# Kernel optimization log

Measured on AMD Instinct MI355X. Metric: run time of the kernel, lower is better.

## Reference

```python
import jax, jax.numpy as jnp
import numpy as np

DIM = 1024
E = 8
TOP_K = 2
HID = int(DIM * 2.68)  # 2744


def setup_inputs() -> dict:
    key = jax.random.key(0)
    ks = jax.random.split(key, 8)
    s = 0.02
    return {
        "x": jax.random.normal(ks[0], (4, 1024, DIM), dtype=jnp.float32),
        "gate_w": jax.random.normal(ks[1], (E, DIM), dtype=jnp.float32) * s,
        "w1": jax.random.normal(ks[2], (E, HID, DIM), dtype=jnp.float32) * s,
        "w2": jax.random.normal(ks[3], (E, HID, DIM), dtype=jnp.float32) * s,
        "w3": jax.random.normal(ks[4], (E, DIM, HID), dtype=jnp.float32) * s,
        "sw1": jax.random.normal(ks[5], (HID, DIM), dtype=jnp.float32) * s,
        "sw2": jax.random.normal(ks[6], (HID, DIM), dtype=jnp.float32) * s,
        "sw3": jax.random.normal(ks[7], (DIM, HID), dtype=jnp.float32) * s,
    }


def reference(x, gate_w, w1, w2, w3, sw1, sw2, sw3):
    B, T, C = x.shape
    xf = x.reshape(-1, C)  # [S, C]
    logits = xf @ gate_w.T  # [S, E]
    rw = jax.nn.softmax(logits.astype(jnp.float32), axis=-1)
    tkw, tki = jax.lax.top_k(rw, TOP_K)  # [S, K]
    nE = rw.shape[-1]
    importance = rw.mean(0)  # [E]
    load = jax.nn.one_hot(tki[:, 0], nE, dtype=jnp.float32).mean(0)  # [E]
    aux_loss = nE * (importance * load).sum()
    tkw = tkw / tkw.sum(-1, keepdims=True)
    tkw = tkw.astype(x.dtype)
    # dense all-expert SwiGLU (faithful to original: every expert on every token)
    h = jax.nn.silu(jnp.einsum('sc,ehc->seh', xf, w1)) * jnp.einsum('sc,ehc->seh', xf, w2)  # [S,E,H]
    eo = jnp.einsum('seh,ech->sec', h, w3)  # [S, E, C]
    sel = jnp.take_along_axis(eo, tki[:, :, None], axis=1)  # [S, K, C]
    weighted = (sel * tkw[:, :, None]).sum(1)  # [S, C]
    shared = (jax.nn.silu(xf @ sw1.T) * (xf @ sw2.T)) @ sw3.T  # [S, C]
    y = (weighted + shared).reshape(B, T, C)
    return y, aux_loss
```

## Files before the change

### kernel.cpp

```cpp
#include <hip/hip_runtime.h>
#include <cstdio>
#include <cstdint>

#define S_TOK 4096
#define CDIM  1024
#define EXP   8
#define HRAW  2744
#define HPAD  2816
#define MAXROWS  13312
#define MAXTILES 104
#define NSLICE1  (HPAD / 128)
#define NSLICE2  (CDIM / 128)

typedef __attribute__((ext_vector_type(8))) short bf16x8;
typedef __attribute__((ext_vector_type(4))) float f32x4;
typedef __attribute__((ext_vector_type(4))) unsigned short us4;
typedef unsigned short us;

__device__ __forceinline__ us f2bf(float f) {
  unsigned u = __float_as_uint(f);
  u += 0x7fffu + ((u >> 16) & 1u);
  return (us)(u >> 16);
}

__device__ __forceinline__ void gl16(const us* g, us* l) {
  __builtin_amdgcn_global_load_lds((__attribute__((address_space(1))) void*)g,
                                   (__attribute__((address_space(3))) void*)l,
                                   16, 0, 0);
}

__device__ __forceinline__ int xcd_swz(int orig, int nwg) {
  int q = nwg >> 3, r = nwg & 7;
  int x = orig & 7, idx = orig >> 3;
  return (x < r ? x * (q + 1) : r * (q + 1) + (x - r) * q) + idx;
}

#define CH_RP1  (HPAD * CDIM / 4)
#define CH_CPR  (HPAD / 4)
#define R_W1    (8 * CH_RP1)
#define R_W2    (R_W1 + 8 * CH_RP1)
#define R_W3    (R_W2 + 8 * CDIM * CH_CPR)
#define R_SW1   (R_W3 + CH_RP1)
#define R_SW2   (R_SW1 + CH_RP1)
#define R_SW3   (R_SW2 + CDIM * CH_CPR)

__device__ __forceinline__ void cvt4_rowpad(const float* __restrict__ src,
                                            us* __restrict__ dst, int idx) {
  int m = idx / CH_RP1, rem = idx - m * CH_RP1;
  int r = rem >> 8, c4 = rem & 255;
  us4 o;
  if (r < HRAW) {
    float4 v = *(const float4*)(src + ((size_t)(m * HRAW + r) * CDIM + c4 * 4));
    o.x = f2bf(v.x); o.y = f2bf(v.y); o.z = f2bf(v.z); o.w = f2bf(v.w);
  } else { o.x = 0; o.y = 0; o.z = 0; o.w = 0; }
  *(us4*)(dst + ((size_t)(m * HPAD + r) * CDIM + c4 * 4)) = o;
}

__device__ __forceinline__ void cvt4_colpad(const float* __restrict__ src,
                                            us* __restrict__ dst, int idx) {
  int r = idx / CH_CPR, c4 = idx - r * CH_CPR;
  int c = c4 * 4;
  us4 o;
  if (c < HRAW) {
    float4 v = *(const float4*)(src + (size_t)r * HRAW + c);
    o.x = f2bf(v.x); o.y = f2bf(v.y); o.z = f2bf(v.z); o.w = f2bf(v.w);
  } else { o.x = 0; o.y = 0; o.z = 0; o.w = 0; }
  *(us4*)(dst + (size_t)r * HPAD + c) = o;
}

__global__ void __launch_bounds__(256) cvt_all_kernel(
    const float* __restrict__ w1, const float* __restrict__ w2,
    const float* __restrict__ w3, const float* __restrict__ sw1,
    const float* __restrict__ sw2, const float* __restrict__ sw3,
    us* __restrict__ w1b, us* __restrict__ w2b, us* __restrict__ w3b,
    us* __restrict__ sw1b, us* __restrict__ sw2b, us* __restrict__ sw3b) {
  for (int i = blockIdx.x * 256 + threadIdx.x; i < R_SW3; i += gridDim.x * 256) {
    if (i < R_W1)       cvt4_rowpad(w1,  w1b,  i);
    else if (i < R_W2)  cvt4_rowpad(w2,  w2b,  i - R_W1);
    else if (i < R_W3)  cvt4_colpad(w3,  w3b,  i - R_W2);
    else if (i < R_SW1) cvt4_rowpad(sw1, sw1b, i - R_W3);
    else if (i < R_SW2) cvt4_rowpad(sw2, sw2b, i - R_SW1);
    else                cvt4_colpad(sw3, sw3b, i - R_SW2);
  }
}

__global__ void __launch_bounds__(256) gate_kernel(const float* __restrict__ x,
                                                   const float* __restrict__ gw,
                                                   us* __restrict__ xb,
                                                   int* __restrict__ tki,
                                                   float* __restrict__ tkw,
                                                   float* __restrict__ probs) {
  const int wv = threadIdx.x >> 6, lane = threadIdx.x & 63;
  const int s = blockIdx.x * 4 + wv;
  const float4* xs4 = (const float4*)(x + (size_t)s * CDIM);
  float acc[8] = {0, 0, 0, 0, 0, 0, 0, 0};
#pragma unroll
  for (int j = 0; j < 4; j++) {
    float4 v = xs4[lane * 4 + j];
    int c = lane * 16 + j * 4;
    us4 ov;
    ov.x = f2bf(v.x); ov.y = f2bf(v.y); ov.z = f2bf(v.z); ov.w = f2bf(v.w);
    *(us4*)(xb + (size_t)s * CDIM + c) = ov;
#pragma unroll
    for (int ee = 0; ee < 8; ee++) {
      const float* g = gw + ee * CDIM + c;
      acc[ee] += v.x * g[0] + v.y * g[1] + v.z * g[2] + v.w * g[3];
    }
  }
#pragma unroll
  for (int ee = 0; ee < 8; ee++) {
#pragma unroll
    for (int off = 32; off > 0; off >>= 1) acc[ee] += __shfl_xor(acc[ee], off, 64);
  }
  if (lane == 0) {
    float mx = acc[0];
    for (int ee = 1; ee < 8; ee++) mx = fmaxf(mx, acc[ee]);
    float p[8], sm = 0.f;
    for (int ee = 0; ee < 8; ee++) { p[ee] = expf(acc[ee] - mx); sm += p[ee]; }
    float inv = 1.f / sm;
    for (int ee = 0; ee < 8; ee++) probs[s * 8 + ee] = p[ee] * inv;
    int i0 = 0; float b0 = p[0];
    for (int ee = 1; ee < 8; ee++) if (p[ee] > b0) { b0 = p[ee]; i0 = ee; }
    int i1 = -1; float b1 = -1.f;
    for (int ee = 0; ee < 8; ee++) if (ee != i0 && p[ee] > b1) { b1 = p[ee]; i1 = ee; }
    float rw0 = b0 * inv, rw1 = b1 * inv;
    float den = 1.f / (rw0 + rw1);
    tki[2 * s] = i0; tki[2 * s + 1] = i1;
    tkw[2 * s] = rw0 * den; tkw[2 * s + 1] = rw1 * den;
  }
}

__global__ void __launch_bounds__(512) build_kernel(const int* __restrict__ tki,
                                                    const float* __restrict__ tkw,
                                                    const float* __restrict__ probs,
                                                    int* __restrict__ meta,
                                                    int* __restrict__ pairtok,
                                                    float* __restrict__ pairw,
                                                    int* __restrict__ invmap,
                                                    int* __restrict__ tile_expert,
                                                    float* __restrict__ aux_out) {
  const int tid = threadIdx.x, lane = tid & 63, wv = tid >> 6;
  __shared__ int s_cnt[EXP];
  __shared__ int s_amc[EXP];
  __shared__ float s_imp[EXP];
  {
    const int e = wv;
    int c_cnt = 0, c_amc = 0;
    float imp = 0.f;
    for (int s0 = 0; s0 < S_TOK; s0 += 64) {
      int s = s0 + lane;
      int i0 = tki[2 * s], i1 = tki[2 * s + 1];
      c_cnt += (i0 == e) || (i1 == e);
      c_amc += (i0 == e);
      imp += probs[s * 8 + e];
    }
#pragma unroll
    for (int off = 32; off > 0; off >>= 1) {
      c_cnt += __shfl_xor(c_cnt, off, 64);
      c_amc += __shfl_xor(c_amc, off, 64);
      imp   += __shfl_xor(imp, off, 64);
    }
    if (lane == 0) { s_cnt[e] = c_cnt; s_amc[e] = c_amc; s_imp[e] = imp; }
  }
  __syncthreads();
  int pad[EXP], start[EXP];
  int o = S_TOK;
#pragma unroll
  for (int j = 0; j < EXP; j++) {
    pad[j] = ((s_cnt[j] + 127) >> 7) << 7;
    start[j] = o;
    o += pad[j];
  }
  const int total = o;
  for (int r = tid; r < S_TOK; r += 512) { pairtok[r] = r; pairw[r] = 1.f; }
  {
    const int e = wv;
    int base = start[e];
    for (int s0 = 0; s0 < S_TOK; s0 += 64) {
      int s = s0 + lane;
      int i0 = tki[2 * s], i1 = tki[2 * s + 1];
      bool m0 = (i0 == e), m1 = (i1 == e);
      bool mm = m0 || m1;
      unsigned long long mk = __ballot(mm);
      if (mm) {
        int pos = base + __popcll(mk & ((1ull << lane) - 1ull));
        pairtok[pos] = s;
        pairw[pos] = m0 ? tkw[2 * s] : tkw[2 * s + 1];
        invmap[2 * s + (m0 ? 0 : 1)] = pos;
      }
      base += __popcll(mk);
    }
    for (int r = base + lane; r < start[e] + pad[e]; r += 64) {
      pairtok[r] = -1; pairw[r] = 0.f;
    }
  }
  if (tid < 128) {
    int ex = 8;
    if (tid >= 32) {
      int rr = tid * 128;
#pragma unroll
      for (int j = 0; j < EXP; j++)
        if (rr >= start[j] && rr < start[j] + pad[j]) ex = j;
    }
    tile_expert[tid] = ex;
  }
  if (tid == 0) {
    meta[0] = total >> 7;
    float a = 0.f;
    for (int j = 0; j < EXP; j++)
      a += (s_imp[j] * (1.f / 4096.f)) * ((float)s_amc[j] * (1.f / 4096.f));
    aux_out[0] = 8.f * a;
  }
}

__global__ void __launch_bounds__(256, 2) gemm1_kernel(
    const us* __restrict__ xb, const us* __restrict__ w1b, const us* __restrict__ w2b,
    const us* __restrict__ sw1b, const us* __restrict__ sw2b,
    const int* __restrict__ pairtok, const int* __restrict__ tile_expert,
    const int* __restrict__ meta, us* __restrict__ h) {
  const int wgid = xcd_swz(blockIdx.x, MAXTILES * NSLICE1);
  const int mt = wgid % MAXTILES;
  if (mt >= meta[0]) return;
  const int n0 = (wgid / MAXTILES) * 128;
  const int e = tile_expert[mt];
  const us* B1 = (e == 8) ? sw1b : (w1b + (size_t)e * HPAD * CDIM);
  const us* B2 = (e == 8) ? sw2b : (w2b + (size_t)e * HPAD * CDIM);
  const int row0 = mt * 128;
  __shared__ __align__(16) us sA[128 * 32];
  __shared__ __align__(16) us sB1[128 * 32];
  __shared__ __align__(16) us sB2[128 * 32];
  const int tid = threadIdx.x, lane = tid & 63;
  const int wm = tid >> 7, wn = (tid >> 6) & 1;
  const int sub = tid & 3, ra = tid >> 2;
  const int subx = sub ^ ((ra >> 1) & 3);
  int t0 = pairtok[row0 + ra];      if (t0 < 0) t0 = 0;
  int t1 = pairtok[row0 + 64 + ra]; if (t1 < 0) t1 = 0;
  const us* gA0 = xb + (size_t)t0 * CDIM + subx * 8;
  const us* gA1 = xb + (size_t)t1 * CDIM + subx * 8;
  const us* gB1a = B1 + (size_t)(n0 + ra) * CDIM + subx * 8;
  const us* gB1b = B1 + (size_t)(n0 + 64 + ra) * CDIM + subx * 8;
  const us* gB2a = B2 + (size_t)(n0 + ra) * CDIM + subx * 8;
  const us* gB2b = B2 + (size_t)(n0 + 64 + ra) * CDIM + subx * 8;
  f32x4 au[4][4], av[4][4];
#pragma unroll
  for (int m = 0; m < 4; m++)
#pragma unroll
    for (int n = 0; n < 4; n++)
#pragma unroll
      for (int r = 0; r < 4; r++) { au[m][n][r] = 0.f; av[m][n][r] = 0.f; }

  const int rl = lane & 15;
  const int kx = (((lane >> 4) ^ ((lane >> 1) & 3)) << 3);
  for (int k0 = 0; k0 < CDIM; k0 += 32) {
    gl16(gA0 + k0,  &sA[tid * 8]);
    gl16(gA1 + k0,  &sA[(tid + 256) * 8]);
    gl16(gB1a + k0, &sB1[tid * 8]);
    gl16(gB1b + k0, &sB1[(tid + 256) * 8]);
    gl16(gB2a + k0, &sB2[tid * 8]);
    gl16(gB2b + k0, &sB2[(tid + 256) * 8]);
    __syncthreads();
    bf16x8 a[4], b1[4], b2[4];
#pragma unroll
    for (int m = 0; m < 4; m++)
      a[m] = *(const bf16x8*)&sA[(wm * 64 + m * 16 + rl) * 32 + kx];
#pragma unroll
    for (int n = 0; n < 4; n++) {
      b1[n] = *(const bf16x8*)&sB1[(wn * 64 + n * 16 + rl) * 32 + kx];
      b2[n] = *(const bf16x8*)&sB2[(wn * 64 + n * 16 + rl) * 32 + kx];
    }
#pragma unroll
    for (int m = 0; m < 4; m++)
#pragma unroll
      for (int n = 0; n < 4; n++) {
        au[m][n] = __builtin_amdgcn_mfma_f32_16x16x32_bf16(a[m], b1[n], au[m][n], 0, 0, 0);
        av[m][n] = __builtin_amdgcn_mfma_f32_16x16x32_bf16(a[m], b2[n], av[m][n], 0, 0, 0);
      }
    __syncthreads();
  }
  const int rb = (lane >> 4) * 4, cb = lane & 15;
#pragma unroll
  for (int m = 0; m < 4; m++)
#pragma unroll
    for (int n = 0; n < 4; n++)
#pragma unroll
      for (int r = 0; r < 4; r++) {
        int row = row0 + wm * 64 + m * 16 + rb + r;
        int col = n0 + wn * 64 + n * 16 + cb;
        float u = au[m][n][r], v = av[m][n][r];
        float sg = 1.f / (1.f + __expf(-u));
        h[(size_t)row * HPAD + col] = f2bf(u * sg * v);
      }
}

__global__ void __launch_bounds__(256, 2) gemm2_kernel(
    const us* __restrict__ h, const us* __restrict__ w3b, const us* __restrict__ sw3b,
    const int* __restrict__ tile_expert, const int* __restrict__ meta,
    float* __restrict__ eo) {
  const int wgid = xcd_swz(blockIdx.x, MAXTILES * NSLICE2);
  const int mt = wgid % MAXTILES;
  if (mt >= meta[0]) return;
  const int n0 = (wgid / MAXTILES) * 128;
  const int e = tile_expert[mt];
  const us* B = (e == 8) ? sw3b : (w3b + (size_t)e * CDIM * HPAD);
  const int row0 = mt * 128;
  __shared__ __align__(16) us sA[128 * 32];
  __shared__ __align__(16) us sB[128 * 32];
  const int tid = threadIdx.x, lane = tid & 63;
  const int wm = tid >> 7, wn = (tid >> 6) & 1;
  const int sub = tid & 3, ra = tid >> 2;
  const int subx = sub ^ ((ra >> 1) & 3);
  const us* gA0 = h + (size_t)(row0 + ra) * HPAD + subx * 8;
  const us* gA1 = h + (size_t)(row0 + 64 + ra) * HPAD + subx * 8;
  const us* gB0 = B + (size_t)(n0 + ra) * HPAD + subx * 8;
  const us* gB1 = B + (size_t)(n0 + 64 + ra) * HPAD + subx * 8;
  f32x4 ac[4][4];
#pragma unroll
  for (int m = 0; m < 4; m++)
#pragma unroll
    for (int n = 0; n < 4; n++)
#pragma unroll
      for (int r = 0; r < 4; r++) ac[m][n][r] = 0.f;

  const int rl = lane & 15;
  const int kx = (((lane >> 4) ^ ((lane >> 1) & 3)) << 3);
  for (int k0 = 0; k0 < HPAD; k0 += 32) {
    gl16(gA0 + k0, &sA[tid * 8]);
    gl16(gA1 + k0, &sA[(tid + 256) * 8]);
    gl16(gB0 + k0, &sB[tid * 8]);
    gl16(gB1 + k0, &sB[(tid + 256) * 8]);
    __syncthreads();
    bf16x8 a[4], b[4];
#pragma unroll
    for (int m = 0; m < 4; m++)
      a[m] = *(const bf16x8*)&sA[(wm * 64 + m * 16 + rl) * 32 + kx];
#pragma unroll
    for (int n = 0; n < 4; n++)
      b[n] = *(const bf16x8*)&sB[(wn * 64 + n * 16 + rl) * 32 + kx];
#pragma unroll
    for (int m = 0; m < 4; m++)
#pragma unroll
      for (int n = 0; n < 4; n++)
        ac[m][n] = __builtin_amdgcn_mfma_f32_16x16x32_bf16(a[m], b[n], ac[m][n], 0, 0, 0);
    __syncthreads();
  }
  const int rb = (lane >> 4) * 4, cb = lane & 15;
#pragma unroll
  for (int m = 0; m < 4; m++)
#pragma unroll
    for (int n = 0; n < 4; n++)
#pragma unroll
      for (int r = 0; r < 4; r++) {
        int row = row0 + wm * 64 + m * 16 + rb + r;
        int col = n0 + wn * 64 + n * 16 + cb;
        eo[(size_t)row * CDIM + col] = ac[m][n][r];
      }
}

__global__ void __launch_bounds__(256) combine_kernel(const float* __restrict__ eo,
                                                      const int* __restrict__ invmap,
                                                      const float* __restrict__ pairw,
                                                      float* __restrict__ out) {
  const int s = blockIdx.x;
  const int c = threadIdx.x * 4;
  const int j0 = invmap[2 * s], j1 = invmap[2 * s + 1];
  const float w0 = pairw[j0], w1 = pairw[j1];
  float4 a = *(const float4*)(eo + (size_t)s * CDIM + c);
  float4 b = *(const float4*)(eo + (size_t)j0 * CDIM + c);
  float4 d = *(const float4*)(eo + (size_t)j1 * CDIM + c);
  float4 o;
  o.x = a.x + w0 * b.x + w1 * d.x;
  o.y = a.y + w0 * b.y + w1 * d.y;
  o.z = a.z + w0 * b.z + w1 * d.z;
  o.w = a.w + w0 * b.w + w1 * d.w;
  *(float4*)(out + (size_t)s * CDIM + c) = o;
}

extern "C" void kernel_launch(void* const* d_in, const int* in_sizes, int n_in,
                              void* d_out, int out_size, void* d_ws, size_t ws_size,
                              hipStream_t stream) {
  const float* x   = (const float*)d_in[0];
  const float* gw  = (const float*)d_in[1];
  const float* w1  = (const float*)d_in[2];
  const float* w2  = (const float*)d_in[3];
  const float* w3  = (const float*)d_in[4];
  const float* sw1 = (const float*)d_in[5];
  const float* sw2 = (const float*)d_in[6];
  const float* sw3 = (const float*)d_in[7];
  float* out = (float*)d_out;
  char* ws = (char*)d_ws;
  size_t off = 0;
  auto take = [&](size_t bytes) -> char* {
    char* p = ws + off;
    off = (off + bytes + 255) & ~(size_t)255;
    return p;
  };
  us* xb    = (us*)take((size_t)S_TOK * CDIM * 2);
  us* w1b   = (us*)take((size_t)EXP * HPAD * CDIM * 2);
  us* w2b   = (us*)take((size_t)EXP * HPAD * CDIM * 2);
  us* w3b   = (us*)take((size_t)EXP * CDIM * HPAD * 2);
  us* sw1b  = (us*)take((size_t)HPAD * CDIM * 2);
  us* sw2b  = (us*)take((size_t)HPAD * CDIM * 2);
  us* sw3b  = (us*)take((size_t)CDIM * HPAD * 2);
  us* hbuf  = (us*)take((size_t)MAXROWS * HPAD * 2);
  int* pairtok = (int*)take(MAXROWS * 4);
  float* pairw = (float*)take(MAXROWS * 4);
  int* invmap  = (int*)take(S_TOK * 2 * 4);
  int* tile_expert = (int*)take(128 * 4);
  int* tki = (int*)take(S_TOK * 2 * 4);
  float* tkw = (float*)take(S_TOK * 2 * 4);
  float* probs = (float*)take(S_TOK * EXP * 4);
  int* meta = (int*)take(256);
  float* eo = (float*)w1b;
  if (off > ws_size) {
    fprintf(stderr, "MoE kernel: ws too small, need %zu got %zu\n", off, ws_size);
    return;
  }
  cvt_all_kernel<<<2048, 256, 0, stream>>>(w1, w2, w3, sw1, sw2, sw3,
                                           w1b, w2b, w3b, sw1b, sw2b, sw3b);
  gate_kernel<<<S_TOK / 4, 256, 0, stream>>>(x, gw, xb, tki, tkw, probs);
  build_kernel<<<1, 512, 0, stream>>>(tki, tkw, probs, meta, pairtok, pairw, invmap,
                                      tile_expert, out + (size_t)S_TOK * CDIM);
  gemm1_kernel<<<MAXTILES * NSLICE1, 256, 0, stream>>>(
      xb, w1b, w2b, sw1b, sw2b, pairtok, tile_expert, meta, hbuf);
  gemm2_kernel<<<MAXTILES * NSLICE2, 256, 0, stream>>>(
      hbuf, w3b, sw3b, tile_expert, meta, eo);
  combine_kernel<<<S_TOK, 256, 0, stream>>>(eo, invmap, pairw, out);
}
```

Before: 470.6 us.

## Pipeline gemm1 with triple-buffered LDS, 512 threads and BK=64

Rewrites the gate/up GEMM kernel to use 8 waves per block with a 3-stage LDS ring buffer and K-step of 64. Global-to-LDS loads for tile t+2 are issued before computing tile t, with vmcnt waits in place of the two full __syncthreads per iteration. A new XOR swizzle on 64-wide rows avoids bank conflicts. This hides memory latency behind MFMA work at the cost of much larger LDS use (144KB) and one block per CU.

```diff
diff --git a/kernel.cpp b/kernel.cpp
--- a/kernel.cpp
+++ b/kernel.cpp
@@ -11,6 +11,8 @@
 #define MAXTILES 104
 #define NSLICE1  (HPAD / 128)
 #define NSLICE2  (CDIM / 128)
+#define NT1K     (CDIM / 64)
+#define NT2      (HPAD / 32)
 
 typedef __attribute__((ext_vector_type(8))) short bf16x8;
 typedef __attribute__((ext_vector_type(4))) float f32x4;
@@ -213,7 +215,7 @@
   }
 }
 
-__global__ void __launch_bounds__(256, 2) gemm1_kernel(
+__global__ void __launch_bounds__(512, 1) gemm1_kernel(
     const us* __restrict__ xb, const us* __restrict__ w1b, const us* __restrict__ w2b,
     const us* __restrict__ sw1b, const us* __restrict__ sw2b,
     const int* __restrict__ pairtok, const int* __restrict__ tile_expert,
@@ -226,66 +228,109 @@
   const us* B1 = (e == 8) ? sw1b : (w1b + (size_t)e * HPAD * CDIM);
   const us* B2 = (e == 8) ? sw2b : (w2b + (size_t)e * HPAD * CDIM);
   const int row0 = mt * 128;
-  __shared__ __align__(16) us sA[128 * 32];
-  __shared__ __align__(16) us sB1[128 * 32];
-  __shared__ __align__(16) us sB2[128 * 32];
-  const int tid = threadIdx.x, lane = tid & 63;
-  const int wm = tid >> 7, wn = (tid >> 6) & 1;
-  const int sub = tid & 3, ra = tid >> 2;
-  const int subx = sub ^ ((ra >> 1) & 3);
-  int t0 = pairtok[row0 + ra];      if (t0 < 0) t0 = 0;
-  int t1 = pairtok[row0 + 64 + ra]; if (t1 < 0) t1 = 0;
-  const us* gA0 = xb + (size_t)t0 * CDIM + subx * 8;
-  const us* gA1 = xb + (size_t)t1 * CDIM + subx * 8;
-  const us* gB1a = B1 + (size_t)(n0 + ra) * CDIM + subx * 8;
-  const us* gB1b = B1 + (size_t)(n0 + 64 + ra) * CDIM + subx * 8;
-  const us* gB2a = B2 + (size_t)(n0 + ra) * CDIM + subx * 8;
-  const us* gB2b = B2 + (size_t)(n0 + 64 + ra) * CDIM + subx * 8;
-  f32x4 au[4][4], av[4][4];
+  __shared__ __align__(16) us sA[3][128 * 64];
+  __shared__ __align__(16) us sB1[3][128 * 64];
+  __shared__ __align__(16) us sB2[3][128 * 64];
+  const int tid = threadIdx.x, lane = tid & 63, wid = tid >> 6;
+  const int wm = wid >> 2, wn = wid & 3;
+  const int srow0 = (wid * 2 + 0) * 8 + (lane >> 3);
+  const int srow1 = (wid * 2 + 1) * 8 + (lane >> 3);
+  const int soct0 = (lane & 7) ^ (srow0 & 7);
+  const int soct1 = (lane & 7) ^ (srow1 & 7);
+  const int ldst0 = (wid * 2 + 0) * 512 + lane * 8;
+  const int ldst1 = (wid * 2 + 1) * 512 + lane * 8;
+  int ta0 = pairtok[row0 + srow0]; if (ta0 < 0) ta0 = 0;
+  int ta1 = pairtok[row0 + srow1]; if (ta1 < 0) ta1 = 0;
+  const us* gA0  = xb + (size_t)ta0 * CDIM + soct0 * 8;
+  const us* gA1  = xb + (size_t)ta1 * CDIM + soct1 * 8;
+  const us* gB1a = B1 + (size_t)(n0 + srow0) * CDIM + soct0 * 8;
+  const us* gB1b = B1 + (size_t)(n0 + srow1) * CDIM + soct1 * 8;
+  const us* gB2a = B2 + (size_t)(n0 + srow0) * CDIM + soct0 * 8;
+  const us* gB2b = B2 + (size_t)(n0 + srow1) * CDIM + soct1 * 8;
+
+#define G1_STAGE(slot, k0)                  \
+  do {                                      \
+    gl16(gA0 + (k0),  &sA[slot][ldst0]);    \
+    gl16(gA1 + (k0),  &sA[slot][ldst1]);    \
+    gl16(gB1a + (k0), &sB1[slot][ldst0]);   \
+    gl16(gB1b + (k0), &sB1[slot][ldst1]);   \
+    gl16(gB2a + (k0), &sB2[slot][ldst0]);   \
+    gl16(gB2b + (k0), &sB2[slot][ldst1]);   \
+  } while (0)
+
+  f32x4 au[4][2], av[4][2];
 #pragma unroll
   for (int m = 0; m < 4; m++)
 #pragma unroll
-    for (int n = 0; n < 4; n++)
+    for (int n = 0; n < 2; n++)
 #pragma unroll
       for (int r = 0; r < 4; r++) { au[m][n][r] = 0.f; av[m][n][r] = 0.f; }
 
-  const int rl = lane & 15;
-  const int kx = (((lane >> 4) ^ ((lane >> 1) & 3)) << 3);
-  for (int k0 = 0; k0 < CDIM; k0 += 32) {
-    gl16(gA0 + k0,  &sA[tid * 8]);
-    gl16(gA1 + k0,  &sA[(tid + 256) * 8]);
-    gl16(gB1a + k0, &sB1[tid * 8]);
-    gl16(gB1b + k0, &sB1[(tid + 256) * 8]);
-    gl16(gB2a + k0, &sB2[tid * 8]);
-    gl16(gB2b + k0, &sB2[(tid + 256) * 8]);
-    __syncthreads();
-    bf16x8 a[4], b1[4], b2[4];
+  const int fr = lane & 15, fo = lane >> 4;
+  int offA[4][2], offB[2][2];
+#pragma unroll
+  for (int m = 0; m < 4; m++)
+#pragma unroll
+    for (int ks = 0; ks < 2; ks++) {
+      int row = wm * 64 + m * 16 + fr;
+      int lo = ks * 4 + fo;
+      offA[m][ks] = row * 64 + (lo ^ (row & 7)) * 8;
+    }
+#pragma unroll
+  for (int n = 0; n < 2; n++)
+#pragma unroll
+    for (int ks = 0; ks < 2; ks++) {
+      int row = wn * 32 + n * 16 + fr;
+      int lo = ks * 4 + fo;
+      offB[n][ks] = row * 64 + (lo ^ (row & 7)) * 8;
+    }
+
+  G1_STAGE(0, 0);
+  G1_STAGE(1, 64);
+#pragma unroll 1
+  for (int t = 0; t < NT1K; t++) {
+    __builtin_amdgcn_sched_barrier(0);
+    __builtin_amdgcn_s_barrier();
+    if (t + 2 < NT1K) G1_STAGE((t + 2) % 3, (t + 2) * 64);
+    if (t < NT1K - 1) asm volatile("s_waitcnt vmcnt(6)" ::: "memory");
+    else              asm volatile("s_waitcnt vmcnt(0)" ::: "memory");
+    __builtin_amdgcn_sched_barrier(0);
+    const us* pa  = sA[t % 3];
+    const us* pb1 = sB1[t % 3];
+    const us* pb2 = sB2[t % 3];
+    bf16x8 a[4][2], b1[2][2], b2[2][2];
 #pragma unroll
     for (int m = 0; m < 4; m++)
-      a[m] = *(const bf16x8*)&sA[(wm * 64 + m * 16 + rl) * 32 + kx];
-#pragma unroll
-    for (int n = 0; n < 4; n++) {
-      b1[n] = *(const bf16x8*)&sB1[(wn * 64 + n * 16 + rl) * 32 + kx];
-      b2[n] = *(const bf16x8*)&sB2[(wn * 64 + n * 16 + rl) * 32 + kx];
-    }
-#pragma unroll
-    for (int m = 0; m < 4; m++)
-#pragma unroll
-      for (int n = 0; n < 4; n++) {
-        au[m][n] = __builtin_amdgcn_mfma_f32_16x16x32_bf16(a[m], b1[n], au[m][n], 0, 0, 0);
-        av[m][n] = __builtin_amdgcn_mfma_f32_16x16x32_bf16(a[m], b2[n], av[m][n], 0, 0, 0);
+#pragma unroll
+      for (int ks = 0; ks < 2; ks++)
+        a[m][ks] = *(const bf16x8*)&pa[offA[m][ks]];
+#pragma unroll
+    for (int n = 0; n < 2; n++)
+#pragma unroll
+      for (int ks = 0; ks < 2; ks++) {
+        b1[n][ks] = *(const bf16x8*)&pb1[offB[n][ks]];
+        b2[n][ks] = *(const bf16x8*)&pb2[offB[n][ks]];
       }
-    __syncthreads();
-  }
+#pragma unroll
+    for (int ks = 0; ks < 2; ks++)
+#pragma unroll
+      for (int m = 0; m < 4; m++)
+#pragma unroll
+        for (int n = 0; n < 2; n++) {
+          au[m][n] = __builtin_amdgcn_mfma_f32_16x16x32_bf16(a[m][ks], b1[n][ks], au[m][n], 0, 0, 0);
+          av[m][n] = __builtin_amdgcn_mfma_f32_16x16x32_bf16(a[m][ks], b2[n][ks], av[m][n], 0, 0, 0);
+        }
+  }
+#undef G1_STAGE
   const int rb = (lane >> 4) * 4, cb = lane & 15;
 #pragma unroll
   for (int m = 0; m < 4; m++)
 #pragma unroll
-    for (int n = 0; n < 4; n++)
+    for (int n = 0; n < 2; n++)
 #pragma unroll
       for (int r = 0; r < 4; r++) {
         int row = row0 + wm * 64 + m * 16 + rb + r;
-        int col = n0 + wn * 64 + n * 16 + cb;
+        int col = n0 + wn * 32 + n * 16 + cb;
         float u = au[m][n][r], v = av[m][n][r];
         float sg = 1.f / (1.f + __expf(-u));
         h[(size_t)row * HPAD + col] = f2bf(u * sg * v);
@@ -420,7 +465,7 @@
   gate_kernel<<<S_TOK / 4, 256, 0, stream>>>(x, gw, xb, tki, tkw, probs);
   build_kernel<<<1, 512, 0, stream>>>(tki, tkw, probs, meta, pairtok, pairw, invmap,
                                       tile_expert, out + (size_t)S_TOK * CDIM);
-  gemm1_kernel<<<MAXTILES * NSLICE1, 256, 0, stream>>>(
+  gemm1_kernel<<<MAXTILES * NSLICE1, 512, 0, stream>>>(
       xb, w1b, w2b, sw1b, sw2b, pairtok, tile_expert, meta, hbuf);
   gemm2_kernel<<<MAXTILES * NSLICE2, 256, 0, stream>>>(
       hbuf, w3b, sw3b, tile_expert, meta, eo);
```

Result: slower. 520.9 us (+10.7%).

## Widen gemm2 N-tile to 256 and merge weight conversion with gating kernel

Applied to the files above, without the earlier changes.

The second GEMM now computes 128x256 output tiles per workgroup instead of 128x128. This halves the grid and reuses each loaded A (h) tile across twice as many columns, cutting global traffic for h. The cost is doubled accumulator registers (128 floats per thread) and a larger B shared buffer, which may lower occupancy or cause spills under the 2-waves launch bound. Separately, the weight-conversion and gating kernels are merged into one launch so the gating blocks run alongside the conversion blocks and one kernel launch is removed.

```diff
diff --git a/kernel.cpp b/kernel.cpp
--- a/kernel.cpp
+++ b/kernel.cpp
@@ -10,7 +10,7 @@
 #define MAXROWS  13312
 #define MAXTILES 104
 #define NSLICE1  (HPAD / 128)
-#define NSLICE2  (CDIM / 128)
+#define NSLICE2  (CDIM / 256)
 
 typedef __attribute__((ext_vector_type(8))) short bf16x8;
 typedef __attribute__((ext_vector_type(4))) float f32x4;
@@ -43,6 +43,8 @@
 #define R_SW1   (R_W3 + CH_RP1)
 #define R_SW2   (R_SW1 + CH_RP1)
 #define R_SW3   (R_SW2 + CDIM * CH_CPR)
+#define GATE_BLKS (S_TOK / 4)
+#define CVT_BLKS  2048
 
 __device__ __forceinline__ void cvt4_rowpad(const float* __restrict__ src,
                                             us* __restrict__ dst, int idx) {
@@ -68,65 +70,64 @@
   *(us4*)(dst + (size_t)r * HPAD + c) = o;
 }
 
-__global__ void __launch_bounds__(256) cvt_all_kernel(
+__global__ void __launch_bounds__(256) cvtgate_kernel(
+    const float* __restrict__ x, const float* __restrict__ gw,
     const float* __restrict__ w1, const float* __restrict__ w2,
     const float* __restrict__ w3, const float* __restrict__ sw1,
     const float* __restrict__ sw2, const float* __restrict__ sw3,
-    us* __restrict__ w1b, us* __restrict__ w2b, us* __restrict__ w3b,
-    us* __restrict__ sw1b, us* __restrict__ sw2b, us* __restrict__ sw3b) {
-  for (int i = blockIdx.x * 256 + threadIdx.x; i < R_SW3; i += gridDim.x * 256) {
-    if (i < R_W1)       cvt4_rowpad(w1,  w1b,  i);
-    else if (i < R_W2)  cvt4_rowpad(w2,  w2b,  i - R_W1);
-    else if (i < R_W3)  cvt4_colpad(w3,  w3b,  i - R_W2);
-    else if (i < R_SW1) cvt4_rowpad(sw1, sw1b, i - R_W3);
-    else if (i < R_SW2) cvt4_rowpad(sw2, sw2b, i - R_SW1);
-    else                cvt4_colpad(sw3, sw3b, i - R_SW2);
-  }
-}
-
-__global__ void __launch_bounds__(256) gate_kernel(const float* __restrict__ x,
-                                                   const float* __restrict__ gw,
-                                                   us* __restrict__ xb,
-                                                   int* __restrict__ tki,
-                                                   float* __restrict__ tkw,
-                                                   float* __restrict__ probs) {
-  const int wv = threadIdx.x >> 6, lane = threadIdx.x & 63;
-  const int s = blockIdx.x * 4 + wv;
-  const float4* xs4 = (const float4*)(x + (size_t)s * CDIM);
-  float acc[8] = {0, 0, 0, 0, 0, 0, 0, 0};
-#pragma unroll
-  for (int j = 0; j < 4; j++) {
-    float4 v = xs4[lane * 4 + j];
-    int c = lane * 16 + j * 4;
-    us4 ov;
-    ov.x = f2bf(v.x); ov.y = f2bf(v.y); ov.z = f2bf(v.z); ov.w = f2bf(v.w);
-    *(us4*)(xb + (size_t)s * CDIM + c) = ov;
+    us* __restrict__ xb, us* __restrict__ w1b, us* __restrict__ w2b,
+    us* __restrict__ w3b, us* __restrict__ sw1b, us* __restrict__ sw2b,
+    us* __restrict__ sw3b, int* __restrict__ tki, float* __restrict__ tkw,
+    float* __restrict__ probs) {
+  if (blockIdx.x < GATE_BLKS) {
+    const int wv = threadIdx.x >> 6, lane = threadIdx.x & 63;
+    const int s = blockIdx.x * 4 + wv;
+    const float4* xs4 = (const float4*)(x + (size_t)s * CDIM);
+    float acc[8] = {0, 0, 0, 0, 0, 0, 0, 0};
+#pragma unroll
+    for (int j = 0; j < 4; j++) {
+      float4 v = xs4[lane * 4 + j];
+      int c = lane * 16 + j * 4;
+      us4 ov;
+      ov.x = f2bf(v.x); ov.y = f2bf(v.y); ov.z = f2bf(v.z); ov.w = f2bf(v.w);
+      *(us4*)(xb + (size_t)s * CDIM + c) = ov;
+#pragma unroll
+      for (int ee = 0; ee < 8; ee++) {
+        const float* g = gw + ee * CDIM + c;
+        acc[ee] += v.x * g[0] + v.y * g[1] + v.z * g[2] + v.w * g[3];
+      }
+    }
 #pragma unroll
     for (int ee = 0; ee < 8; ee++) {
-      const float* g = gw + ee * CDIM + c;
-      acc[ee] += v.x * g[0] + v.y * g[1] + v.z * g[2] + v.w * g[3];
-    }
-  }
-#pragma unroll
-  for (int ee = 0; ee < 8; ee++) {
-#pragma unroll
-    for (int off = 32; off > 0; off >>= 1) acc[ee] += __shfl_xor(acc[ee], off, 64);
-  }
-  if (lane == 0) {
-    float mx = acc[0];
-    for (int ee = 1; ee < 8; ee++) mx = fmaxf(mx, acc[ee]);
-    float p[8], sm = 0.f;
-    for (int ee = 0; ee < 8; ee++) { p[ee] = expf(acc[ee] - mx); sm += p[ee]; }
-    float inv = 1.f / sm;
-    for (int ee = 0; ee < 8; ee++) probs[s * 8 + ee] = p[ee] * inv;
-    int i0 = 0; float b0 = p[0];
-    for (int ee = 1; ee < 8; ee++) if (p[ee] > b0) { b0 = p[ee]; i0 = ee; }
-    int i1 = -1; float b1 = -1.f;
-    for (int ee = 0; ee < 8; ee++) if (ee != i0 && p[ee] > b1) { b1 = p[ee]; i1 = ee; }
-    float rw0 = b0 * inv, rw1 = b1 * inv;
-    float den = 1.f / (rw0 + rw1);
-    tki[2 * s] = i0; tki[2 * s + 1] = i1;
-    tkw[2 * s] = rw0 * den; tkw[2 * s + 1] = rw1 * den;
+#pragma unroll
+      for (int off = 32; off > 0; off >>= 1) acc[ee] += __shfl_xor(acc[ee], off, 64);
+    }
+    if (lane == 0) {
+      float mx = acc[0];
+      for (int ee = 1; ee < 8; ee++) mx = fmaxf(mx, acc[ee]);
+      float p[8], sm = 0.f;
+      for (int ee = 0; ee < 8; ee++) { p[ee] = expf(acc[ee] - mx); sm += p[ee]; }
+      float inv = 1.f / sm;
+      for (int ee = 0; ee < 8; ee++) probs[s * 8 + ee] = p[ee] * inv;
+      int i0 = 0; float b0 = p[0];
+      for (int ee = 1; ee < 8; ee++) if (p[ee] > b0) { b0 = p[ee]; i0 = ee; }
+      int i1 = -1; float b1 = -1.f;
+      for (int ee = 0; ee < 8; ee++) if (ee != i0 && p[ee] > b1) { b1 = p[ee]; i1 = ee; }
+      float rw0 = b0 * inv, rw1 = b1 * inv;
+      float den = 1.f / (rw0 + rw1);
+      tki[2 * s] = i0; tki[2 * s + 1] = i1;
+      tkw[2 * s] = rw0 * den; tkw[2 * s + 1] = rw1 * den;
+    }
+  } else {
+    for (int i = (blockIdx.x - GATE_BLKS) * 256 + threadIdx.x; i < R_SW3;
+         i += CVT_BLKS * 256) {
+      if (i < R_W1)       cvt4_rowpad(w1,  w1b,  i);
+      else if (i < R_W2)  cvt4_rowpad(w2,  w2b,  i - R_W1);
+      else if (i < R_W3)  cvt4_colpad(w3,  w3b,  i - R_W2);
+      else if (i < R_SW1) cvt4_rowpad(sw1, sw1b, i - R_W3);
+      else if (i < R_SW2) cvt4_rowpad(sw2, sw2b, i - R_SW1);
+      else                cvt4_colpad(sw3, sw3b, i - R_SW2);
+    }
   }
 }
 
@@ -299,12 +300,12 @@
   const int wgid = xcd_swz(blockIdx.x, MAXTILES * NSLICE2);
   const int mt = wgid % MAXTILES;
   if (mt >= meta[0]) return;
-  const int n0 = (wgid / MAXTILES) * 128;
+  const int n0 = (wgid / MAXTILES) * 256;
   const int e = tile_expert[mt];
   const us* B = (e == 8) ? sw3b : (w3b + (size_t)e * CDIM * HPAD);
   const int row0 = mt * 128;
   __shared__ __align__(16) us sA[128 * 32];
-  __shared__ __align__(16) us sB[128 * 32];
+  __shared__ __align__(16) us sB[256 * 32];
   const int tid = threadIdx.x, lane = tid & 63;
   const int wm = tid >> 7, wn = (tid >> 6) & 1;
   const int sub = tid & 3, ra = tid >> 2;
@@ -313,11 +314,13 @@
   const us* gA1 = h + (size_t)(row0 + 64 + ra) * HPAD + subx * 8;
   const us* gB0 = B + (size_t)(n0 + ra) * HPAD + subx * 8;
   const us* gB1 = B + (size_t)(n0 + 64 + ra) * HPAD + subx * 8;
-  f32x4 ac[4][4];
+  const us* gB2 = B + (size_t)(n0 + 128 + ra) * HPAD + subx * 8;
+  const us* gB3 = B + (size_t)(n0 + 192 + ra) * HPAD + subx * 8;
+  f32x4 ac[4][8];
 #pragma unroll
   for (int m = 0; m < 4; m++)
 #pragma unroll
-    for (int n = 0; n < 4; n++)
+    for (int n = 0; n < 8; n++)
 #pragma unroll
       for (int r = 0; r < 4; r++) ac[m][n][r] = 0.f;
 
@@ -328,18 +331,20 @@
     gl16(gA1 + k0, &sA[(tid + 256) * 8]);
     gl16(gB0 + k0, &sB[tid * 8]);
     gl16(gB1 + k0, &sB[(tid + 256) * 8]);
+    gl16(gB2 + k0, &sB[(tid + 512) * 8]);
+    gl16(gB3 + k0, &sB[(tid + 768) * 8]);
     __syncthreads();
-    bf16x8 a[4], b[4];
+    bf16x8 a[4], b[8];
 #pragma unroll
     for (int m = 0; m < 4; m++)
       a[m] = *(const bf16x8*)&sA[(wm * 64 + m * 16 + rl) * 32 + kx];
 #pragma unroll
-    for (int n = 0; n < 4; n++)
-      b[n] = *(const bf16x8*)&sB[(wn * 64 + n * 16 + rl) * 32 + kx];
+    for (int n = 0; n < 8; n++)
+      b[n] = *(const bf16x8*)&sB[(wn * 128 + n * 16 + rl) * 32 + kx];
 #pragma unroll
     for (int m = 0; m < 4; m++)
 #pragma unroll
-      for (int n = 0; n < 4; n++)
+      for (int n = 0; n < 8; n++)
         ac[m][n] = __builtin_amdgcn_mfma_f32_16x16x32_bf16(a[m], b[n], ac[m][n], 0, 0, 0);
     __syncthreads();
   }
@@ -347,11 +352,11 @@
 #pragma unroll
   for (int m = 0; m < 4; m++)
 #pragma unroll
-    for (int n = 0; n < 4; n++)
+    for (int n = 0; n < 8; n++)
 #pragma unroll
       for (int r = 0; r < 4; r++) {
         int row = row0 + wm * 64 + m * 16 + rb + r;
-        int col = n0 + wn * 64 + n * 16 + cb;
+        int col = n0 + wn * 128 + n * 16 + cb;
         eo[(size_t)row * CDIM + col] = ac[m][n][r];
       }
 }
@@ -415,9 +420,9 @@
     fprintf(stderr, "MoE kernel: ws too small, need %zu got %zu\n", off, ws_size);
     return;
   }
-  cvt_all_kernel<<<2048, 256, 0, stream>>>(w1, w2, w3, sw1, sw2, sw3,
-                                           w1b, w2b, w3b, sw1b, sw2b, sw3b);
-  gate_kernel<<<S_TOK / 4, 256, 0, stream>>>(x, gw, xb, tki, tkw, probs);
+  cvtgate_kernel<<<GATE_BLKS + CVT_BLKS, 256, 0, stream>>>(
+      x, gw, w1, w2, w3, sw1, sw2, sw3,
+      xb, w1b, w2b, w3b, sw1b, sw2b, sw3b, tki, tkw, probs);
   build_kernel<<<1, 512, 0, stream>>>(tki, tkw, probs, meta, pairtok, pairw, invmap,
                                       tile_expert, out + (size_t)S_TOK * CDIM);
   gemm1_kernel<<<MAXTILES * NSLICE1, 256, 0, stream>>>(
```

Measured after the change: 472.0 us. No clear change (+0.3%).
